# Kernel tuning notes

Measured on AMD Instinct MI355X. Metric: run time of the kernel, lower is better.

The kernel has to match this reference:

```python
import jax, jax.numpy as jnp
import numpy as np
import math

B, N, DEG, C, F0, NCLS = 128, 512, 8, 128, 128, 10
E = B * N * DEG
RATIO = 0.8
K1 = math.ceil(RATIO * N)    # 410
K2 = math.ceil(RATIO * K1)   # 328
K3 = math.ceil(RATIO * K2)   # 263


def setup_inputs() -> dict:
    key = jax.random.key(0)
    ks = jax.random.split(key, 32)
    x = jax.random.normal(ks[0], (B * N, F0), jnp.float32)
    epg = N * DEG
    src_l = jax.random.randint(ks[1], (B, epg), 0, N)
    dst_l = jax.random.randint(ks[2], (B, epg), 0, N)
    off = (jnp.arange(B, dtype=jnp.int32) * N)[:, None]
    edge_src = (src_l + off).reshape(-1).astype(jnp.int32)
    edge_dst = (dst_l + off).reshape(-1).astype(jnp.int32)

    def lin(k, fi, fo):
        return jax.random.normal(k, (fi, fo), jnp.float32) / np.float32(np.sqrt(fi))

    inp = {"x": x, "edge_src": edge_src, "edge_dst": edge_dst}
    i = 3
    for s, fi in (("1", F0), ("2", C), ("3", C)):
        inp["Wroot" + s] = lin(ks[i], fi, C); i += 1
        inp["Wrel" + s] = lin(ks[i], fi, C); i += 1
        inp["brel" + s] = jnp.zeros((C,), jnp.float32)
        inp["p" + s] = jax.random.normal(ks[i], (C,), jnp.float32); i += 1
    inp["W1"] = lin(ks[i], 2 * C, 128); i += 1
    inp["b1"] = jnp.zeros((128,), jnp.float32)
    inp["W2"] = lin(ks[i], 128, 64); i += 1
    inp["b2"] = jnp.zeros((64,), jnp.float32)
    inp["W3"] = lin(ks[i], 64, NCLS); i += 1
    inp["b3"] = jnp.zeros((NCLS,), jnp.float32)
    return inp


def graph_conv(x, src, dst, emask, Wroot, Wrel, brel, num_nodes):
    # PyG GraphConv (aggr='add'): lin_rel(sum_j x_j) + lin_root(x_i)
    msg = x[src] * emask[:, None]                      # masked gather  [E, C]
    agg = jax.ops.segment_sum(msg, dst, num_segments=num_nodes)
    return agg @ Wrel + brel + x @ Wroot


def topk_pool(x, p, src, dst, emask, b, n, k):
    # score = tanh(x . p / ||p||), keep top-k nodes per graph, scale kept x by score
    score = jnp.tanh((x @ p) / jnp.linalg.norm(p))     # [b*n]
    vals, idx = jax.lax.top_k(score.reshape(b, n), k)  # [b, k]
    perm = (idx + (jnp.arange(b, dtype=idx.dtype) * n)[:, None]).reshape(-1)
    x_new = x[perm] * vals.reshape(-1, 1)
    inv = jnp.full((b * n,), -1, jnp.int32).at[perm].set(
        jnp.arange(b * k, dtype=jnp.int32))
    ns, nd = inv[src], inv[dst]
    nmask = emask * (ns >= 0) * (nd >= 0)
    return x_new, jnp.maximum(ns, 0), jnp.maximum(nd, 0), nmask


def readout(h, b, k):
    hb = h.reshape(b, k, -1)
    return jnp.concatenate([hb.max(axis=1), hb.mean(axis=1)], axis=-1)  # gmp||gap


def reference(x, edge_src, edge_dst,
              Wroot1, Wrel1, brel1, p1,
              Wroot2, Wrel2, brel2, p2,
              Wroot3, Wrel3, brel3, p3,
              W1, b1, W2, b2, W3, b3):
    emask = jnp.ones((E,), x.dtype)
    s, d = edge_src, edge_dst

    h = jax.nn.relu(graph_conv(x, s, d, emask, Wroot1, Wrel1, brel1, B * N))
    h, s, d, emask = topk_pool(h, p1, s, d, emask, B, N, K1)
    x1 = readout(h, B, K1)

    h = jax.nn.relu(graph_conv(h, s, d, emask, Wroot2, Wrel2, brel2, B * K1))
    h, s, d, emask = topk_pool(h, p2, s, d, emask, B, K1, K2)
    x2 = readout(h, B, K2)

    h = jax.nn.relu(graph_conv(h, s, d, emask, Wroot3, Wrel3, brel3, B * K2))
    h, s, d, emask = topk_pool(h, p3, s, d, emask, B, K2, K3)
    x3 = readout(h, B, K3)

    g = x1 + x2 + x3                                   # [B, 256]
    g = jax.nn.relu(g @ W1 + b1)                       # dropout is identity in eval
    g = jax.nn.relu(g @ W2 + b2)
    return jax.nn.log_softmax(g @ W3 + b3, axis=-1)    # [B, NCLS]
```

## Files before the change

### kernel.cpp

```cpp
#include <hip/hip_runtime.h>
#include <hip/hip_bf16.h>
#include <math.h>

#define B_G   128
#define N0    512
#define DEG   8
#define CCH   128
#define EPG   (N0*DEG)
#define E_TOTAL (B_G*EPG)
#define K1    410
#define K2    328
#define K3    263
#define NCLS  10

using bf16x8 = __attribute__((ext_vector_type(8))) __bf16;
using f32x4  = __attribute__((ext_vector_type(4))) float;
typedef unsigned short ushort;
typedef unsigned int uint;

__device__ __forceinline__ ushort f2b(float f) {
    uint u = __float_as_uint(f);
    u += 0x7fffu + ((u >> 16) & 1u);
    return (ushort)(u >> 16);
}
__device__ __forceinline__ float b2f(ushort h) {
    return __uint_as_float(((uint)h) << 16);
}
__device__ __forceinline__ void split2(float v, ushort& hi, ushort& lo) {
    hi = f2b(v);
    lo = f2b(v - b2f(hi));
}
__device__ __forceinline__ uint pksplit(float v) {
    ushort h, l; split2(v, h, l);
    return (uint)h | ((uint)l << 16);
}
__device__ __forceinline__ float unpk(uint u) {
    return __uint_as_float(u << 16) + __uint_as_float(u & 0xffff0000u);
}

__global__ void convert_x(const float* __restrict__ x0, uint* __restrict__ xp, int n4) {
    int i = blockIdx.x * 256 + threadIdx.x;
    if (i >= n4) return;
    float4 v = ((const float4*)x0)[i];
    uint4 o;
    o.x = pksplit(v.x); o.y = pksplit(v.y); o.z = pksplit(v.z); o.w = pksplit(v.w);
    ((uint4*)xp)[i] = o;
}

__global__ void pack_weights(const float* __restrict__ Wrel0, const float* __restrict__ Wroot0,
                             const float* __restrict__ Wrel1, const float* __restrict__ Wroot1,
                             const float* __restrict__ Wrel2, const float* __restrict__ Wroot2,
                             ushort* __restrict__ Bph, ushort* __restrict__ Bpl) {
    int idx = blockIdx.x * 256 + threadIdx.x;
    if (idx >= 3 * 32768) return;
    int layer = idx >> 15, rem = idx & 32767;
    int j = rem & 7, lane = (rem >> 3) & 63, cf = (rem >> 9) & 7, ks = rem >> 12;
    int k = ks * 32 + (lane >> 4) * 8 + j;
    int c = cf * 16 + (lane & 15);
    const float* Wrel  = layer == 0 ? Wrel0  : layer == 1 ? Wrel1  : Wrel2;
    const float* Wroot = layer == 0 ? Wroot0 : layer == 1 ? Wroot1 : Wroot2;
    float v = (k < 128) ? Wrel[k * 128 + c] : Wroot[(k - 128) * 128 + c];
    ushort hi, lo; split2(v, hi, lo);
    Bph[idx] = hi; Bpl[idx] = lo;
}

__global__ void init_all(int* __restrict__ mapT, float* __restrict__ gpart) {
    int i = blockIdx.x * 256 + threadIdx.x;
    if (i < B_G * N0) mapT[i] = i;
    if (i < 3 * 4 * B_G * 256) gpart[i] = 0.f;
}

__global__ __launch_bounds__(512) void csr_build(
        const int* __restrict__ es, const int* __restrict__ ed, const int* __restrict__ mapT,
        int* __restrict__ indptr, int* __restrict__ counts, int* __restrict__ srclist,
        int n_cur) {
    int b = blockIdx.x, tid = threadIdx.x;
    __shared__ int mloc[512];
    __shared__ int cnt[512];
    __shared__ int pref[512];
    __shared__ int curs[512];
    __shared__ uint epk[EPG];
    mloc[tid] = mapT[b * N0 + tid];
    cnt[tid] = 0;
    __syncthreads();
    int base = b * EPG;
    int nb = b * n_cur;
    for (int i = tid; i < EPG; i += 512) {
        int s = es[base + i] & (N0 - 1);
        int d = ed[base + i] & (N0 - 1);
        int sg = mloc[s], dg = mloc[d];
        uint wv = 0xFFFFFFFFu;
        if ((sg | dg) >= 0) {
            int sl = sg - nb, dl = dg - nb;
            wv = (uint)sl | ((uint)dl << 16);
            atomicAdd(&cnt[dl], 1);
        }
        epk[i] = wv;
    }
    __syncthreads();
    pref[tid] = cnt[tid];
    __syncthreads();
    for (int off = 1; off < 512; off <<= 1) {
        int v = (tid >= off) ? pref[tid - off] : 0;
        __syncthreads();
        pref[tid] += v;
        __syncthreads();
    }
    int excl = tid ? pref[tid - 1] : 0;
    if (tid < n_cur) {
        indptr[nb + tid] = base + excl;
        counts[nb + tid] = cnt[tid];
    }
    curs[tid] = excl;
    __syncthreads();
    for (int i = tid; i < EPG; i += 512) {
        uint wv = epk[i];
        if (wv != 0xFFFFFFFFu) {
            int dl = wv >> 16;
            int pos = atomicAdd(&curs[dl], 1);
            srclist[base + pos] = (int)(wv & 0xFFFFu);
        }
    }
}

__global__ __launch_bounds__(1024) void aggregate(
        const uint* __restrict__ xp,
        const int* __restrict__ indptr, const int* __restrict__ counts,
        const int* __restrict__ srclist,
        uint* __restrict__ aggp, int n) {
    extern __shared__ float slab[];
    int b = blockIdx.x >> 2, q = blockIdx.x & 3;
    int tid = threadIdx.x;
    for (int t = tid; t < n * 32; t += 1024) {
        int nd = t >> 5, ch = t & 31;
        uint u = xp[(size_t)(b * n + nd) * CCH + q * 32 + ch];
        slab[nd * 32 + ch] = unpk(u);
    }
    __syncthreads();
    int wave = tid >> 6, lane = tid & 63;
    int gl = lane >> 3;
    int sub = lane & 7;
    int ngroups = (n + 7) >> 3;
    for (int g = wave; g < ngroups; g += 16) {
        int d = g * 8 + gl;
        bool act = d < n;
        int beg = 0, cnt = 0;
        if (act) { beg = indptr[b * n + d]; cnt = counts[b * n + d]; }
        float4 acc = make_float4(0.f, 0.f, 0.f, 0.f);
        int id_next = (cnt > 0) ? srclist[beg] : 0;
        for (int j = 0; j < cnt; j++) {
            int id = id_next;
            if (j + 1 < cnt) id_next = srclist[beg + j + 1];
            const float4 v = *(const float4*)&slab[id * 32 + sub * 4];
            acc.x += v.x; acc.y += v.y; acc.z += v.z; acc.w += v.w;
        }
        if (act) {
            uint4 o;
            o.x = pksplit(acc.x); o.y = pksplit(acc.y);
            o.z = pksplit(acc.z); o.w = pksplit(acc.w);
            *(uint4*)&aggp[(size_t)(b * n + d) * CCH + q * 32 + sub * 4] = o;
        }
    }
}

__global__ __launch_bounds__(512, 4) void transform_mfma(
        const uint* __restrict__ aggp, const uint* __restrict__ xp,
        const ushort* __restrict__ Bph, const ushort* __restrict__ Bpl,
        const float* __restrict__ brel, const float* __restrict__ pvec,
        uint* __restrict__ hp, float* __restrict__ score) {
    __shared__ ushort ldsBh[16384];
    __shared__ ushort ldsBl[16384];
    int tid = threadIdx.x;
    int wave = tid >> 6, lane = tid & 63;
    int r = lane & 15, kb = lane >> 4;
    int rows0 = blockIdx.x * 128 + wave * 16;

    f32x4 acc[8];
#pragma unroll
    for (int cf = 0; cf < 8; cf++) acc[cf] = (f32x4)(0.f);

    union U16 { uint u[4]; bf16x8 v; };

#pragma unroll
    for (int half = 0; half < 2; half++) {
        if (half) __syncthreads();
#pragma unroll
        for (int i = 0; i < 4; i++) {
            int idx = tid + i * 512;
            ((uint4*)ldsBh)[idx] = ((const uint4*)(Bph + half * 16384))[idx];
            ((uint4*)ldsBl)[idx] = ((const uint4*)(Bpl + half * 16384))[idx];
        }
        __syncthreads();
        const uint* A = half ? xp : aggp;
#pragma unroll
        for (int ks4 = 0; ks4 < 4; ks4++) {
            size_t rowbase = (size_t)(rows0 + r) * CCH + ks4 * 32 + kb * 8;
            uint4 ua = *(const uint4*)&A[rowbase];
            uint4 ub = *(const uint4*)&A[rowbase + 4];
            U16 ah, al;
            ah.u[0] = (ua.x & 0xffffu) | (ua.y << 16);
            ah.u[1] = (ua.z & 0xffffu) | (ua.w << 16);
            ah.u[2] = (ub.x & 0xffffu) | (ub.y << 16);
            ah.u[3] = (ub.z & 0xffffu) | (ub.w << 16);
            al.u[0] = (ua.x >> 16) | (ua.y & 0xffff0000u);
            al.u[1] = (ua.z >> 16) | (ua.w & 0xffff0000u);
            al.u[2] = (ub.x >> 16) | (ub.y & 0xffff0000u);
            al.u[3] = (ub.z >> 16) | (ub.w & 0xffff0000u);
#pragma unroll
            for (int cf = 0; cf < 8; cf++) {
                bf16x8 bh = *(const bf16x8*)&ldsBh[((ks4 * 8 + cf) * 64 + lane) * 8];
                bf16x8 bl = *(const bf16x8*)&ldsBl[((ks4 * 8 + cf) * 64 + lane) * 8];
                acc[cf] = __builtin_amdgcn_mfma_f32_16x16x32_bf16(ah.v, bl, acc[cf], 0, 0, 0);
                acc[cf] = __builtin_amdgcn_mfma_f32_16x16x32_bf16(al.v, bh, acc[cf], 0, 0, 0);
                acc[cf] = __builtin_amdgcn_mfma_f32_16x16x32_bf16(ah.v, bh, acc[cf], 0, 0, 0);
            }
        }
    }

    float pv[8], bb[8], q = 0.f;
#pragma unroll
    for (int cf = 0; cf < 8; cf++) {
        pv[cf] = pvec[cf * 16 + r];
        bb[cf] = brel[cf * 16 + r];
        q += pv[cf] * pv[cf];
    }
    float dots[4] = {0.f, 0.f, 0.f, 0.f};
#pragma unroll
    for (int cf = 0; cf < 8; cf++) {
#pragma unroll
        for (int reg = 0; reg < 4; reg++) {
            float v = acc[cf][reg] + bb[cf];
            v = v > 0.f ? v : 0.f;
            hp[(size_t)(rows0 + kb * 4 + reg) * CCH + cf * 16 + r] = pksplit(v);
            dots[reg] += v * pv[cf];
        }
    }
#pragma unroll
    for (int off = 1; off < 16; off <<= 1) {
        q += __shfl_xor(q, off);
#pragma unroll
        for (int reg = 0; reg < 4; reg++) dots[reg] += __shfl_xor(dots[reg], off);
    }
    if (r == 0) {
        float inv_norm = rsqrtf(q);
#pragma unroll
        for (int reg = 0; reg < 4; reg++)
            score[rows0 + kb * 4 + reg] = tanhf(dots[reg] * inv_norm);
    }
}

__global__ __launch_bounds__(512) void pool_kernel(
        const float* __restrict__ score, const uint* __restrict__ hp,
        uint* __restrict__ xp, float* __restrict__ gpart, int* __restrict__ mapT,
        int n, int k, int layer, int last) {
    int b = blockIdx.x >> 2, q = blockIdx.x & 3;
    int tid = threadIdx.x;
    __shared__ unsigned long long keys[512];
    __shared__ short invl[512];
    __shared__ float wmax[8][128], wsum[8][128];
    {
        unsigned long long key = 0ull;
        if (tid < n) {
            uint u = __float_as_uint(score[b * n + tid]);
            u = (u & 0x80000000u) ? ~u : (u | 0x80000000u);
            key = ((unsigned long long)u << 32) | (uint)(~tid);
        }
        keys[tid] = key;
        invl[tid] = -1;
    }
    __syncthreads();
    for (int kk2 = 2; kk2 <= 512; kk2 <<= 1) {
        for (int j = kk2 >> 1; j > 0; j >>= 1) {
            int s = tid, sxj = s ^ j;
            if (sxj > s) {
                unsigned long long a = keys[s], c = keys[sxj];
                bool doSwap = ((s & kk2) == 0) ? (a < c) : (a > c);
                if (doSwap) { keys[s] = c; keys[sxj] = a; }
            }
            __syncthreads();
        }
    }
    if (tid < k) {
        int node = (int)(~(uint)keys[tid]);
        invl[node] = (short)tid;
    }
    __syncthreads();
    int wave = tid >> 6, lane = tid & 63;
    float mx0 = -1e30f, mx1 = -1e30f, sm0 = 0.f, sm1 = 0.f;
    for (int j = q + 4 * wave; j < k; j += 32) {
        unsigned long long key = keys[j];
        int node = (int)(~(uint)key);
        uint tu = (uint)(key >> 32);
        uint su = (tu & 0x80000000u) ? (tu & 0x7fffffffu) : ~tu;
        float v = __uint_as_float(su);
        uint2 u = ((const uint2*)(hp + (size_t)(b * n + node) * CCH))[lane];
        float c0 = unpk(u.x) * v;
        float c1 = unpk(u.y) * v;
        ((uint2*)(xp + (size_t)(b * k + j) * CCH))[lane] = make_uint2(pksplit(c0), pksplit(c1));
        mx0 = fmaxf(mx0, c0); sm0 += c0;
        mx1 = fmaxf(mx1, c1); sm1 += c1;
    }
    wmax[wave][2 * lane] = mx0; wmax[wave][2 * lane + 1] = mx1;
    wsum[wave][2 * lane] = sm0; wsum[wave][2 * lane + 1] = sm1;
    __syncthreads();
    if (tid < 128) {
        float m = wmax[0][tid], s = wsum[0][tid];
#pragma unroll
        for (int w = 1; w < 8; w++) { m = fmaxf(m, wmax[w][tid]); s += wsum[w][tid]; }
        float* gp = gpart + ((size_t)(layer * 4 + q) * B_G + b) * 256;
        gp[tid] = m;
        gp[128 + tid] = s;
    }
    if (!last && q == 0) {
        int m = mapT[b * N0 + tid];
        int res = -1;
        if (m >= 0) {
            int nl = invl[m - b * n];
            if (nl >= 0) res = b * k + nl;
        }
        mapT[b * N0 + tid] = res;
    }
}

__global__ __launch_bounds__(128) void mlp_kernel(const float* __restrict__ gpart,
        const float* __restrict__ W1, const float* __restrict__ b1,
        const float* __restrict__ W2, const float* __restrict__ b2,
        const float* __restrict__ W3, const float* __restrict__ b3,
        float* __restrict__ out) {
    int b = blockIdx.x, t = threadIdx.x;
    __shared__ float gs[256], h1[128], h2[64], lg[10];
    const float kdiv[3] = {(float)K1, (float)K2, (float)K3};
    float a0 = 0.f, a1 = 0.f;
#pragma unroll
    for (int l = 0; l < 3; l++) {
        float m = -1e30f, s = 0.f;
#pragma unroll
        for (int q = 0; q < 4; q++) {
            const float* gp = gpart + ((size_t)(l * 4 + q) * B_G + b) * 256;
            m = fmaxf(m, gp[t]);
            s += gp[128 + t];
        }
        a0 += m;
        a1 += s / kdiv[l];
    }
    gs[t] = a0;
    gs[128 + t] = a1;
    __syncthreads();
    {
        float a = b1[t];
        for (int c = 0; c < 256; c++) a += gs[c] * W1[c * 128 + t];
        h1[t] = fmaxf(a, 0.f);
    }
    __syncthreads();
    if (t < 64) {
        float a = b2[t];
        for (int c = 0; c < 128; c++) a += h1[c] * W2[c * 64 + t];
        h2[t] = fmaxf(a, 0.f);
    }
    __syncthreads();
    if (t < 10) {
        float a = b3[t];
        for (int c = 0; c < 64; c++) a += h2[c] * W3[c * 10 + t];
        lg[t] = a;
    }
    __syncthreads();
    if (t < 10) {
        float m = lg[0];
        for (int i = 1; i < 10; i++) m = fmaxf(m, lg[i]);
        float s = 0.f;
        for (int i = 0; i < 10; i++) s += expf(lg[i] - m);
        out[b * 10 + t] = lg[t] - m - logf(s);
    }
}

extern "C" void kernel_launch(void* const* d_in, const int* in_sizes, int n_in,
                              void* d_out, int out_size, void* d_ws, size_t ws_size,
                              hipStream_t stream) {
    (void)in_sizes; (void)n_in; (void)out_size; (void)ws_size;
    const float* x0 = (const float*)d_in[0];
    const int* es = (const int*)d_in[1];
    const int* ed = (const int*)d_in[2];
    const float* Wroot[3] = {(const float*)d_in[3], (const float*)d_in[7], (const float*)d_in[11]};
    const float* Wrel[3]  = {(const float*)d_in[4], (const float*)d_in[8], (const float*)d_in[12]};
    const float* brel[3]  = {(const float*)d_in[5], (const float*)d_in[9], (const float*)d_in[13]};
    const float* pvec[3]  = {(const float*)d_in[6], (const float*)d_in[10], (const float*)d_in[14]};
    const float* W1 = (const float*)d_in[15];
    const float* b1 = (const float*)d_in[16];
    const float* W2 = (const float*)d_in[17];
    const float* b2 = (const float*)d_in[18];
    const float* W3 = (const float*)d_in[19];
    const float* b3 = (const float*)d_in[20];

    size_t off = 0;
    char* base = (char*)d_ws;
    auto alloc = [&](size_t bytes) -> void* {
        void* p = base + off;
        off += (bytes + 255) & ~(size_t)255;
        return p;
    };
    const size_t FEATP = (size_t)(B_G * N0) * CCH * 4;
    uint* xp   = (uint*)alloc(FEATP);
    uint* aggp = (uint*)alloc(FEATP);
    ushort* Bph = (ushort*)alloc((size_t)3 * 32768 * 2);
    ushort* Bpl = (ushort*)alloc((size_t)3 * 32768 * 2);
    int* mapT   = (int*)alloc((size_t)(B_G * N0) * 4);
    int* counts = (int*)alloc((size_t)(B_G * N0) * 4);
    int* indptr = (int*)alloc((size_t)(B_G * N0) * 4);
    int* srclist = (int*)alloc((size_t)E_TOTAL * 4);
    float* score = (float*)alloc((size_t)(B_G * N0) * 4);
    float* gpart = (float*)alloc((size_t)3 * 4 * B_G * 256 * 4);

    convert_x<<<(B_G * N0 * CCH / 4 + 255) / 256, 256, 0, stream>>>(x0, xp,
                                                                    B_G * N0 * CCH / 4);
    pack_weights<<<(3 * 32768 + 255) / 256, 256, 0, stream>>>(
        Wrel[0], Wroot[0], Wrel[1], Wroot[1], Wrel[2], Wroot[2], Bph, Bpl);
    init_all<<<(3 * 4 * B_G * 256 + 255) / 256, 256, 0, stream>>>(mapT, gpart);

    int nper[4] = {N0, K1, K2, K3};
    for (int l = 0; l < 3; l++) {
        int n = nper[l], k = nper[l + 1];
        int n_nodes = B_G * n;
        csr_build<<<B_G, 512, 0, stream>>>(es, ed, mapT, indptr, counts, srclist, n);
        aggregate<<<4 * B_G, 1024, (size_t)n * 32 * 4, stream>>>(
            xp, indptr, counts, srclist, aggp, n);
        transform_mfma<<<n_nodes / 128, 512, 0, stream>>>(
            aggp, xp, Bph + (size_t)l * 32768, Bpl + (size_t)l * 32768,
            brel[l], pvec[l], aggp, score);
        pool_kernel<<<4 * B_G, 512, 0, stream>>>(score, aggp, xp, gpart, mapT, n, k, l, l == 2);
    }
    mlp_kernel<<<B_G, 128, 0, stream>>>(gpart, W1, b1, W2, b2, W3, b3, (float*)d_out);
}
```

Baseline: 234.5 us.

## Fuse CSR rebuild into pool kernel and merge prep launches

Merges the input conversion, weight packing and init kernels into one prep kernel. It adds a dedicated first-layer CSR kernel with no masking. Later CSR rebuilds are folded into the pool kernel: block q==0 rebuilds the CSR while the other three blocks per graph do the gather, scale and readout. The aggregate slab load is also vectorized to uint4. This removes several kernel launches, but the pool kernel now needs much more shared memory (a 16KB edge buffer), which may reduce occupancy and leaves the readout work split unevenly across blocks.

```diff
diff --git a/kernel.cpp b/kernel.cpp
--- a/kernel.cpp
+++ b/kernel.cpp
@@ -38,88 +38,67 @@
     return __uint_as_float(u << 16) + __uint_as_float(u & 0xffff0000u);
 }
 
-__global__ void convert_x(const float* __restrict__ x0, uint* __restrict__ xp, int n4) {
+__global__ void prep_kernel(const float* __restrict__ x0, uint* __restrict__ xp, int n4,
+                            const float* __restrict__ Wrel0, const float* __restrict__ Wroot0,
+                            const float* __restrict__ Wrel1, const float* __restrict__ Wroot1,
+                            const float* __restrict__ Wrel2, const float* __restrict__ Wroot2,
+                            ushort* __restrict__ Bph, ushort* __restrict__ Bpl) {
     int i = blockIdx.x * 256 + threadIdx.x;
-    if (i >= n4) return;
-    float4 v = ((const float4*)x0)[i];
-    uint4 o;
-    o.x = pksplit(v.x); o.y = pksplit(v.y); o.z = pksplit(v.z); o.w = pksplit(v.w);
-    ((uint4*)xp)[i] = o;
-}
-
-__global__ void pack_weights(const float* __restrict__ Wrel0, const float* __restrict__ Wroot0,
-                             const float* __restrict__ Wrel1, const float* __restrict__ Wroot1,
-                             const float* __restrict__ Wrel2, const float* __restrict__ Wroot2,
-                             ushort* __restrict__ Bph, ushort* __restrict__ Bpl) {
-    int idx = blockIdx.x * 256 + threadIdx.x;
-    if (idx >= 3 * 32768) return;
-    int layer = idx >> 15, rem = idx & 32767;
-    int j = rem & 7, lane = (rem >> 3) & 63, cf = (rem >> 9) & 7, ks = rem >> 12;
-    int k = ks * 32 + (lane >> 4) * 8 + j;
-    int c = cf * 16 + (lane & 15);
-    const float* Wrel  = layer == 0 ? Wrel0  : layer == 1 ? Wrel1  : Wrel2;
-    const float* Wroot = layer == 0 ? Wroot0 : layer == 1 ? Wroot1 : Wroot2;
-    float v = (k < 128) ? Wrel[k * 128 + c] : Wroot[(k - 128) * 128 + c];
-    ushort hi, lo; split2(v, hi, lo);
-    Bph[idx] = hi; Bpl[idx] = lo;
-}
-
-__global__ void init_all(int* __restrict__ mapT, float* __restrict__ gpart) {
-    int i = blockIdx.x * 256 + threadIdx.x;
-    if (i < B_G * N0) mapT[i] = i;
-    if (i < 3 * 4 * B_G * 256) gpart[i] = 0.f;
-}
-
-__global__ __launch_bounds__(512) void csr_build(
-        const int* __restrict__ es, const int* __restrict__ ed, const int* __restrict__ mapT,
-        int* __restrict__ indptr, int* __restrict__ counts, int* __restrict__ srclist,
-        int n_cur) {
+    if (i < n4) {
+        float4 v = ((const float4*)x0)[i];
+        uint4 o;
+        o.x = pksplit(v.x); o.y = pksplit(v.y); o.z = pksplit(v.z); o.w = pksplit(v.w);
+        ((uint4*)xp)[i] = o;
+    }
+    if (i < 3 * 32768) {
+        int layer = i >> 15, rem = i & 32767;
+        int j = rem & 7, lane = (rem >> 3) & 63, cf = (rem >> 9) & 7, ks = rem >> 12;
+        int k = ks * 32 + (lane >> 4) * 8 + j;
+        int c = cf * 16 + (lane & 15);
+        const float* Wrel  = layer == 0 ? Wrel0  : layer == 1 ? Wrel1  : Wrel2;
+        const float* Wroot = layer == 0 ? Wroot0 : layer == 1 ? Wroot1 : Wroot2;
+        float v = (k < 128) ? Wrel[k * 128 + c] : Wroot[(k - 128) * 128 + c];
+        ushort hi, lo; split2(v, hi, lo);
+        Bph[i] = hi; Bpl[i] = lo;
+    }
+}
+
+__global__ __launch_bounds__(1024) void csr0_kernel(
+        const int* __restrict__ es, const int* __restrict__ ed, int* __restrict__ mapT,
+        int* __restrict__ indptr, int* __restrict__ counts, int* __restrict__ srclist) {
     int b = blockIdx.x, tid = threadIdx.x;
-    __shared__ int mloc[512];
-    __shared__ int cnt[512];
-    __shared__ int pref[512];
-    __shared__ int curs[512];
     __shared__ uint epk[EPG];
-    mloc[tid] = mapT[b * N0 + tid];
-    cnt[tid] = 0;
+    __shared__ int cnt[512], pref[512], curs[512];
+    if (tid < 512) { cnt[tid] = 0; mapT[b * N0 + tid] = b * N0 + tid; }
     __syncthreads();
     int base = b * EPG;
-    int nb = b * n_cur;
-    for (int i = tid; i < EPG; i += 512) {
+    for (int i = tid; i < EPG; i += 1024) {
         int s = es[base + i] & (N0 - 1);
         int d = ed[base + i] & (N0 - 1);
-        int sg = mloc[s], dg = mloc[d];
-        uint wv = 0xFFFFFFFFu;
-        if ((sg | dg) >= 0) {
-            int sl = sg - nb, dl = dg - nb;
-            wv = (uint)sl | ((uint)dl << 16);
-            atomicAdd(&cnt[dl], 1);
-        }
-        epk[i] = wv;
-    }
-    __syncthreads();
-    pref[tid] = cnt[tid];
+        epk[i] = (uint)s | ((uint)d << 16);
+        atomicAdd(&cnt[d], 1);
+    }
+    __syncthreads();
+    if (tid < 512) pref[tid] = cnt[tid];
     __syncthreads();
     for (int off = 1; off < 512; off <<= 1) {
-        int v = (tid >= off) ? pref[tid - off] : 0;
-        __syncthreads();
-        pref[tid] += v;
-        __syncthreads();
-    }
-    int excl = tid ? pref[tid - 1] : 0;
-    if (tid < n_cur) {
-        indptr[nb + tid] = base + excl;
-        counts[nb + tid] = cnt[tid];
-    }
-    curs[tid] = excl;
-    __syncthreads();
-    for (int i = tid; i < EPG; i += 512) {
+        int v = (tid >= off && tid < 512) ? pref[tid - off] : 0;
+        __syncthreads();
+        if (tid < 512) pref[tid] += v;
+        __syncthreads();
+    }
+    if (tid < 512) {
+        int excl = tid ? pref[tid - 1] : 0;
+        indptr[b * N0 + tid] = base + excl;
+        counts[b * N0 + tid] = cnt[tid];
+        curs[tid] = excl;
+    }
+    __syncthreads();
+    for (int i = tid; i < EPG; i += 1024) {
         uint wv = epk[i];
-        if (wv != 0xFFFFFFFFu) {
-            int dl = wv >> 16;
-            int pos = atomicAdd(&curs[dl], 1);
-            srclist[base + pos] = (int)(wv & 0xFFFFu);
-        }
+        int dl = wv >> 16;
+        int pos = atomicAdd(&curs[dl], 1);
+        srclist[base + pos] = (int)(wv & 0xFFFFu);
     }
 }
 
@@ -131,10 +110,11 @@
     extern __shared__ float slab[];
     int b = blockIdx.x >> 2, q = blockIdx.x & 3;
     int tid = threadIdx.x;
-    for (int t = tid; t < n * 32; t += 1024) {
-        int nd = t >> 5, ch = t & 31;
-        uint u = xp[(size_t)(b * n + nd) * CCH + q * 32 + ch];
-        slab[nd * 32 + ch] = unpk(u);
+    for (int t = tid; t < n * 8; t += 1024) {
+        int nd = t >> 3, c4 = t & 7;
+        uint4 u = *(const uint4*)&xp[(size_t)(b * n + nd) * CCH + q * 32 + c4 * 4];
+        *(float4*)&slab[nd * 32 + c4 * 4] =
+            make_float4(unpk(u.x), unpk(u.y), unpk(u.z), unpk(u.w));
     }
     __syncthreads();
     int wave = tid >> 6, lane = tid & 63;
@@ -252,12 +232,17 @@
 __global__ __launch_bounds__(512) void pool_kernel(
         const float* __restrict__ score, const uint* __restrict__ hp,
         uint* __restrict__ xp, float* __restrict__ gpart, int* __restrict__ mapT,
+        const int* __restrict__ es, const int* __restrict__ ed,
+        int* __restrict__ indptr, int* __restrict__ counts, int* __restrict__ srclist,
         int n, int k, int layer, int last) {
     int b = blockIdx.x >> 2, q = blockIdx.x & 3;
     int tid = threadIdx.x;
     __shared__ unsigned long long keys[512];
     __shared__ short invl[512];
     __shared__ float wmax[8][128], wsum[8][128];
+    __shared__ int newmap[512];
+    __shared__ uint epk[EPG];
+    __shared__ int cnt[512], pref[512], curs[512];
     {
         unsigned long long key = 0ull;
         if (tid < n) {
@@ -285,33 +270,9 @@
         invl[node] = (short)tid;
     }
     __syncthreads();
-    int wave = tid >> 6, lane = tid & 63;
-    float mx0 = -1e30f, mx1 = -1e30f, sm0 = 0.f, sm1 = 0.f;
-    for (int j = q + 4 * wave; j < k; j += 32) {
-        unsigned long long key = keys[j];
-        int node = (int)(~(uint)key);
-        uint tu = (uint)(key >> 32);
-        uint su = (tu & 0x80000000u) ? (tu & 0x7fffffffu) : ~tu;
-        float v = __uint_as_float(su);
-        uint2 u = ((const uint2*)(hp + (size_t)(b * n + node) * CCH))[lane];
-        float c0 = unpk(u.x) * v;
-        float c1 = unpk(u.y) * v;
-        ((uint2*)(xp + (size_t)(b * k + j) * CCH))[lane] = make_uint2(pksplit(c0), pksplit(c1));
-        mx0 = fmaxf(mx0, c0); sm0 += c0;
-        mx1 = fmaxf(mx1, c1); sm1 += c1;
-    }
-    wmax[wave][2 * lane] = mx0; wmax[wave][2 * lane + 1] = mx1;
-    wsum[wave][2 * lane] = sm0; wsum[wave][2 * lane + 1] = sm1;
-    __syncthreads();
-    if (tid < 128) {
-        float m = wmax[0][tid], s = wsum[0][tid];
-#pragma unroll
-        for (int w = 1; w < 8; w++) { m = fmaxf(m, wmax[w][tid]); s += wsum[w][tid]; }
-        float* gp = gpart + ((size_t)(layer * 4 + q) * B_G + b) * 256;
-        gp[tid] = m;
-        gp[128 + tid] = s;
-    }
-    if (!last && q == 0) {
+
+    if (q == 0) {
+        if (last) return;
         int m = mapT[b * N0 + tid];
         int res = -1;
         if (m >= 0) {
@@ -319,6 +280,76 @@
             if (nl >= 0) res = b * k + nl;
         }
         mapT[b * N0 + tid] = res;
+        newmap[tid] = res;
+        cnt[tid] = 0;
+        __syncthreads();
+        int base = b * EPG;
+        int nb = b * k;
+        for (int i = tid; i < EPG; i += 512) {
+            int s = es[base + i] & (N0 - 1);
+            int d = ed[base + i] & (N0 - 1);
+            int sg = newmap[s], dg = newmap[d];
+            uint wv = 0xFFFFFFFFu;
+            if ((sg | dg) >= 0) {
+                int sl = sg - nb, dl = dg - nb;
+                wv = (uint)sl | ((uint)dl << 16);
+                atomicAdd(&cnt[dl], 1);
+            }
+            epk[i] = wv;
+        }
+        __syncthreads();
+        pref[tid] = cnt[tid];
+        __syncthreads();
+        for (int off = 1; off < 512; off <<= 1) {
+            int v = (tid >= off) ? pref[tid - off] : 0;
+            __syncthreads();
+            pref[tid] += v;
+            __syncthreads();
+        }
+        int excl = tid ? pref[tid - 1] : 0;
+        if (tid < k) {
+            indptr[nb + tid] = base + excl;
+            counts[nb + tid] = cnt[tid];
+        }
+        curs[tid] = excl;
+        __syncthreads();
+        for (int i = tid; i < EPG; i += 512) {
+            uint wv = epk[i];
+            if (wv != 0xFFFFFFFFu) {
+                int dl = wv >> 16;
+                int pos = atomicAdd(&curs[dl], 1);
+                srclist[base + pos] = (int)(wv & 0xFFFFu);
+            }
+        }
+    } else {
+        int p = q - 1;
+        int wave = tid >> 6, lane = tid & 63;
+        float mx0 = -1e30f, mx1 = -1e30f, sm0 = 0.f, sm1 = 0.f;
+        for (int j = p + 3 * wave; j < k; j += 24) {
+            unsigned long long key = keys[j];
+            int node = (int)(~(uint)key);
+            uint tu = (uint)(key >> 32);
+            uint su = (tu & 0x80000000u) ? (tu & 0x7fffffffu) : ~tu;
+            float v = __uint_as_float(su);
+            uint2 u = ((const uint2*)(hp + (size_t)(b * n + node) * CCH))[lane];
+            float c0 = unpk(u.x) * v;
+            float c1 = unpk(u.y) * v;
+            ((uint2*)(xp + (size_t)(b * k + j) * CCH))[lane] =
+                make_uint2(pksplit(c0), pksplit(c1));
+            mx0 = fmaxf(mx0, c0); sm0 += c0;
+            mx1 = fmaxf(mx1, c1); sm1 += c1;
+        }
+        wmax[wave][2 * lane] = mx0; wmax[wave][2 * lane + 1] = mx1;
+        wsum[wave][2 * lane] = sm0; wsum[wave][2 * lane + 1] = sm1;
+        __syncthreads();
+        if (tid < 128) {
+            float m = wmax[0][tid], s = wsum[0][tid];
+#pragma unroll
+            for (int w = 1; w < 8; w++) { m = fmaxf(m, wmax[w][tid]); s += wsum[w][tid]; }
+            float* gp = gpart + ((size_t)(layer * 3 + p) * B_G + b) * 256;
+            gp[tid] = m;
+            gp[128 + tid] = s;
+        }
     }
 }
 
@@ -335,8 +366,8 @@
     for (int l = 0; l < 3; l++) {
         float m = -1e30f, s = 0.f;
 #pragma unroll
-        for (int q = 0; q < 4; q++) {
-            const float* gp = gpart + ((size_t)(l * 4 + q) * B_G + b) * 256;
+        for (int p = 0; p < 3; p++) {
+            const float* gp = gpart + ((size_t)(l * 3 + p) * B_G + b) * 256;
             m = fmaxf(m, gp[t]);
             s += gp[128 + t];
         }
@@ -408,25 +439,25 @@
     int* indptr = (int*)alloc((size_t)(B_G * N0) * 4);
     int* srclist = (int*)alloc((size_t)E_TOTAL * 4);
     float* score = (float*)alloc((size_t)(B_G * N0) * 4);
-    float* gpart = (float*)alloc((size_t)3 * 4 * B_G * 256 * 4);
-
-    convert_x<<<(B_G * N0 * CCH / 4 + 255) / 256, 256, 0, stream>>>(x0, xp,
-                                                                    B_G * N0 * CCH / 4);
-    pack_weights<<<(3 * 32768 + 255) / 256, 256, 0, stream>>>(
-        Wrel[0], Wroot[0], Wrel[1], Wroot[1], Wrel[2], Wroot[2], Bph, Bpl);
-    init_all<<<(3 * 4 * B_G * 256 + 255) / 256, 256, 0, stream>>>(mapT, gpart);
+    float* gpart = (float*)alloc((size_t)3 * 3 * B_G * 256 * 4);
+
+    const int N4 = B_G * N0 * CCH / 4;
+    prep_kernel<<<(N4 + 255) / 256, 256, 0, stream>>>(
+        x0, xp, N4, Wrel[0], Wroot[0], Wrel[1], Wroot[1], Wrel[2], Wroot[2], Bph, Bpl);
+    csr0_kernel<<<B_G, 1024, 0, stream>>>(es, ed, mapT, indptr, counts, srclist);
 
     int nper[4] = {N0, K1, K2, K3};
     for (int l = 0; l < 3; l++) {
         int n = nper[l], k = nper[l + 1];
         int n_nodes = B_G * n;
-        csr_build<<<B_G, 512, 0, stream>>>(es, ed, mapT, indptr, counts, srclist, n);
         aggregate<<<4 * B_G, 1024, (size_t)n * 32 * 4, stream>>>(
             xp, indptr, counts, srclist, aggp, n);
         transform_mfma<<<n_nodes / 128, 512, 0, stream>>>(
             aggp, xp, Bph + (size_t)l * 32768, Bpl + (size_t)l * 32768,
             brel[l], pvec[l], aggp, score);
-        pool_kernel<<<4 * B_G, 512, 0, stream>>>(score, aggp, xp, gpart, mapT, n, k, l, l == 2);
+        pool_kernel<<<4 * B_G, 512, 0, stream>>>(
+            score, aggp, xp, gpart, mapT, es, ed, indptr, counts, srclist,
+            n, k, l, l == 2);
     }
     mlp_kernel<<<B_G, 128, 0, stream>>>(gpart, W1, b1, W2, b2, W3, b3, (float*)d_out);
 }
```

Result: faster. 219.5 us (-6.4%).
